# Kernel optimization log

Measured on AMD Instinct MI355X. Metric: run time of the kernel, lower is better.

Reference implementation:

```python
import jax, jax.numpy as jnp
import numpy as np

EPS = 1e-6
NEG = -100000.0


def _ln(x):
    # LayerNorm, elementwise_affine=False, eps=1e-6
    mu = jnp.mean(x, axis=-1, keepdims=True)
    var = jnp.mean((x - mu) ** 2, axis=-1, keepdims=True)
    return (x - mu) * jax.lax.rsqrt(var + EPS)


def _split_heads(x, h):
    b, s, d = x.shape
    return x.reshape(b, s, h, d // h).transpose(0, 2, 1, 3)  # [B,H,S,Dh]


def _merge_heads(x):
    b, h, s, dh = x.shape
    return x.transpose(0, 2, 1, 3).reshape(b, s, h * dh)


def _conv_pool(x, w):
    # grouped Conv2d(num_heads -> num_heads, kernel=(4,1), stride=(4,1), groups=num_heads, bias=False)
    # x: [B,H,S,Dh] as NCHW, w: [H,1,4,1] as OIHW
    return jax.lax.conv_general_dilated(
        x, w, window_strides=(4, 1), padding='VALID',
        dimension_numbers=('NCHW', 'OIHW', 'NCHW'),
        feature_group_count=x.shape[1])


def setup_inputs() -> dict:
    key = jax.random.key(0)
    ks = jax.random.split(key, 14)
    B, S, M, D, QKV, MLP, H = 4, 4096, 256, 768, 768, 3072, 12
    std = 0.02
    f = lambda k, shp: jax.random.normal(k, shp, jnp.float32) * std
    return {
        'x': jax.random.normal(ks[0], (B, S, D), jnp.float32),
        'memory': jax.random.normal(ks[1], (B, M, D), jnp.float32),
        'mask': jax.random.randint(ks[2], (B, S), 0, 2).astype(jnp.int32),
        'Wq': f(ks[3], (QKV, D)), 'Wk': f(ks[4], (QKV, D)),
        'Wv': f(ks[5], (QKV, D)), 'Wo': f(ks[6], (D, QKV)),
        'conv_w': f(ks[7], (H, 1, 4, 1)),
        'Uq': f(ks[8], (QKV, D)), 'Uk': f(ks[9], (QKV, D)),
        'Uv': f(ks[10], (QKV, D)), 'Uo': f(ks[11], (D, QKV)),
        'W1': f(ks[12], (MLP, D)), 'W2': f(ks[13], (D, MLP)),
    }


def reference(x, memory, mask, Wq, Wk, Wv, Wo, conv_w, Uq, Uk, Uv, Uo, W1, W2):
    H = conv_w.shape[0]
    maskf = mask.astype(x.dtype)                       # [B,S]

    # ---- pack: ConvAttention(memory as q, x as k/v); conv downsamples k/v ->
    #      shape_change=True so the k_mask is skipped (as in the torch code).
    q = _split_heads(memory @ Wq.T, H)                 # [B,H,M,Dh], unit temperature (log_temp=0)
    k = _split_heads(x @ Wk.T, H)                      # [B,H,S,Dh]
    v = _split_heads(x @ Wv.T, H)
    k = _conv_pool(k, conv_w)                          # [B,H,S//4,Dh]
    v = _conv_pool(v, conv_w)
    logits = jnp.einsum('bhqd,bhkd->bhqk', q, k)
    att = jax.nn.softmax(logits, axis=-1)
    packed = _merge_heads(att @ v) @ Wo.T              # [B,M,D]

    # ---- unpack: TAttention(x as q, packed as k/v) with q_mask injection
    head_dim = Uq.shape[0] // H
    uq = _split_heads(x @ Uq.T, H) * (1.0 / jnp.sqrt(jnp.asarray(head_dim, x.dtype)))
    uk = _split_heads(packed @ Uk.T, H)                # [B,H,M,Dh]
    uv = _split_heads(packed @ Uv.T, H)
    ulogits = jnp.einsum('bhqd,bhkd->bhqk', uq, uk)    # [B,H,S,M]
    ulogits = ulogits + NEG * (1.0 - maskf[:, None, :, None])
    uatt = jax.nn.softmax(ulogits, axis=-1)
    unpacked = _merge_heads(uatt @ uv) @ Uo.T          # [B,S,D]

    unpacked = unpacked * maskf[..., None]
    q_out = _ln(x + unpacked)
    m_out = _ln(memory + packed)

    # FFN: Linear -> GELU(exact) -> Linear (dropout=0)
    h = jax.nn.gelu(jnp.einsum('bsd,md->bsm', q_out, W1), approximate=False)
    y = jnp.einsum('bsm,dm->bsd', h, W2)
    y = y * maskf[..., None]
    q_out = _ln(q_out + y)
    return (q_out, m_out)
```

## Files before the change

### kernel.cpp

```cpp
#include <hip/hip_runtime.h>
#include <hip/hip_bf16.h>
#include <math.h>


typedef unsigned short u16;
typedef __attribute__((ext_vector_type(8))) short bf8v;
typedef __attribute__((ext_vector_type(4))) float f4v;
typedef __attribute__((ext_vector_type(4))) unsigned short us4v;

#define AS1 __attribute__((address_space(1)))
#define AS3 __attribute__((address_space(3)))

__device__ __forceinline__ void gld_lds16(const void* g, void* l) {
  __builtin_amdgcn_global_load_lds((const AS1 unsigned int*)g,
                                   (AS3 unsigned int*)l, 16, 0, 0);
}

__device__ __forceinline__ u16 bf16_rne(float x) {
  unsigned u = __float_as_uint(x);
  return (u16)((u + 0x7fffu + ((u >> 16) & 1u)) >> 16);
}
__device__ __forceinline__ float bf16_to_f(u16 h) {
  return __uint_as_float(((unsigned)h) << 16);
}

struct Cvt8 {
  const float* src[8];
  u16* dst[8];
  int n4[8];
  float sc[8];
  int cum[9];
  int ns;
};
__global__ __launch_bounds__(256) void tobf16_multi_kernel(Cvt8 c) {
  int b = blockIdx.x;
  int seg = 0;
  while (seg + 1 < c.ns && b >= c.cum[seg + 1]) ++seg;
  int i = (b - c.cum[seg]) * 256 + threadIdx.x;
  if (i >= c.n4[seg]) return;
  const float sc = c.sc[seg];
  float4 v = ((const float4*)c.src[seg])[i];
  us4v h;
  h[0] = bf16_rne(v.x * sc); h[1] = bf16_rne(v.y * sc);
  h[2] = bf16_rne(v.z * sc); h[3] = bf16_rne(v.w * sc);
  ((us4v*)c.dst[seg])[i] = h;
}

template <int BN, int GELU, int OMODE>
__global__ __launch_bounds__(256) void bgemm_kernel(
    const u16* __restrict__ A, const u16* __restrict__ B,
    float* __restrict__ Cf, u16* __restrict__ Cb, int M, int N, int K,
    int lda, int ldb, int ldc, long long aSB, long long aSH, long long bSB,
    long long bSH, long long cSB, long long cSH, int HB, float scale) {
  constexpr int NJ = BN / 32;
  constexpr int LPB = BN / 64;
  __shared__ u16 smA[2][4096];
  __shared__ u16 smB[2][BN * 32];
  const int t = threadIdx.x;
  const int w = t >> 6, lane = t & 63;
  const int z = blockIdx.z;
  const int bb = z / HB, hh = z % HB;
  const u16* Ab = A + bb * aSB + hh * aSH;
  const u16* Bb = B + bb * bSB + hh * bSH;
  float* Cfb = (OMODE != 1) ? (Cf + bb * cSB + hh * cSH) : nullptr;
  u16* Cbb = (OMODE >= 1) ? (Cb + bb * cSB + hh * cSH) : nullptr;

  const int gx = gridDim.x;
  const int nwg = gx * gridDim.y;
  int f = blockIdx.x + gx * blockIdx.y;
  if ((nwg & 7) == 0) {
    const int cpx = nwg >> 3;
    f = (f & 7) * cpx + (f >> 3);
  }
  const int row0 = (f / gx) * 128, col0 = (f % gx) * BN;

  const int brow_l = lane >> 2;
  const int bchunk = ((lane & 3) ^ ((lane >> 3) & 3)) * 8;
  const int fr = lane & 15;
  const int fq = lane >> 4;
  const int fco = (fq ^ ((lane >> 1) & 3)) * 8;
  const int wr = (w >> 1) * 64, wc = (w & 1) * (BN / 2);

  f4v acc[4][NJ];
#pragma unroll
  for (int i = 0; i < 4; ++i)
#pragma unroll
    for (int j = 0; j < NJ; ++j) acc[i][j] = {0.f, 0.f, 0.f, 0.f};

  const int NT = K >> 5;

#pragma unroll
  for (int i = 0; i < 2; ++i) {
    const int g = w * 2 + i;
    const int r = g * 16 + brow_l;
    gld_lds16(Ab + (long long)(row0 + r) * lda + bchunk,
              &smA[0][g * 512 + lane * 8]);
  }
#pragma unroll
  for (int i = 0; i < LPB; ++i) {
    const int g = w * LPB + i;
    const int r = g * 16 + brow_l;
    gld_lds16(Bb + (long long)(col0 + r) * ldb + bchunk,
              &smB[0][g * 512 + lane * 8]);
  }
  __syncthreads();

  for (int tt = 0; tt < NT; ++tt) {
    const int cur = tt & 1, nxt = cur ^ 1;
    const bool more = (tt + 1) < NT;
    if (more) {
      const int k1 = (tt + 1) << 5;
#pragma unroll
      for (int i = 0; i < 2; ++i) {
        const int g = w * 2 + i;
        const int r = g * 16 + brow_l;
        gld_lds16(Ab + (long long)(row0 + r) * lda + k1 + bchunk,
                  &smA[nxt][g * 512 + lane * 8]);
      }
#pragma unroll
      for (int i = 0; i < LPB; ++i) {
        const int g = w * LPB + i;
        const int r = g * 16 + brow_l;
        gld_lds16(Bb + (long long)(col0 + r) * ldb + k1 + bchunk,
                  &smB[nxt][g * 512 + lane * 8]);
      }
    }
    {
      bf8v af[4], bfr[NJ];
#pragma unroll
      for (int mi = 0; mi < 4; ++mi)
        af[mi] = *(const bf8v*)&smA[cur][(wr + mi * 16 + fr) * 32 + fco];
#pragma unroll
      for (int nj = 0; nj < NJ; ++nj)
        bfr[nj] = *(const bf8v*)&smB[cur][(wc + nj * 16 + fr) * 32 + fco];
#pragma unroll
      for (int mi = 0; mi < 4; ++mi)
#pragma unroll
        for (int nj = 0; nj < NJ; ++nj)
          acc[mi][nj] = __builtin_amdgcn_mfma_f32_16x16x32_bf16(
              af[mi], bfr[nj], acc[mi][nj], 0, 0, 0);
    }
    __syncthreads();
  }

#pragma unroll
  for (int mi = 0; mi < 4; ++mi)
#pragma unroll
    for (int nj = 0; nj < NJ; ++nj) {
      const int col = col0 + wc + nj * 16 + fr;
      const long long base =
          (long long)(row0 + wr + mi * 16 + fq * 4) * ldc + col;
#pragma unroll
      for (int j = 0; j < 4; ++j) {
        float v = acc[mi][nj][j] * scale;
        if (GELU) v = 0.5f * v * (1.f + erff(v * 0.70710678118654752f));
        const long long idx = base + (long long)j * ldc;
        if (OMODE != 1) Cfb[idx] = v;
        if (OMODE >= 1) Cbb[idx] = bf16_rne(v);
      }
    }
}

__global__ __launch_bounds__(512) void fused_pack_attn(
    const u16* __restrict__ q, const u16* __restrict__ k,
    const u16* __restrict__ vt, u16* __restrict__ o) {
  __shared__ char pool[110080];
  u16* smQ = (u16*)pool;
  u16* smK = (u16*)(pool + 16384);
  u16* Pbuf = (u16*)(pool + 32768);
  u16* smV = (u16*)(pool + 98304);
  float* partial = (float*)(pool + 106496);
  float* mold = (float*)(pool + 108544);
  float* fbuf = (float*)(pool + 109056);
  float* srow = (float*)(pool + 109568);

  const int t = threadIdx.x;
  const int w = t >> 6, lane = t & 63;
  const int z = blockIdx.z;
  const int b = z / 12, h = z % 12;
  const int qrow0 = b * 256 + blockIdx.x * 128;
  const long long kvbase = ((long long)(b * 12 + h)) * 65536;

  const int fr = lane & 15, fq = lane >> 4;
  const int fco = (fq ^ ((lane >> 1) & 3)) * 8;
  const int brow_l = lane >> 2;
  const int bchunk = ((lane & 3) ^ ((lane >> 3) & 3)) * 8;
  const int wr = (w >> 2) * 64, wc = (w & 3) * 64;
  const int wrp = (w >> 1) * 32, wcp = (w & 1) * 32;

#pragma unroll
  for (int i = 0; i < 2; ++i) {
    const int g = w * 2 + i;
    const int plane = g >> 3, grp = g & 7;
    gld_lds16(q + (long long)(qrow0 + grp * 16 + brow_l) * 768 + h * 64 +
                  plane * 32 + bchunk,
              smQ + plane * 4096 + grp * 512 + lane * 8);
  }
  if (t < 128) {
    mold[t] = -3.0e38f;
    srow[t] = 0.f;
  }

  f4v acc2[2][2];
#pragma unroll
  for (int i = 0; i < 2; ++i)
#pragma unroll
    for (int j = 0; j < 2; ++j) acc2[i][j] = {0.f, 0.f, 0.f, 0.f};

  for (int kc = 0; kc < 4; ++kc) {
    f4v acc[4][4];
#pragma unroll
    for (int i = 0; i < 4; ++i)
#pragma unroll
      for (int j = 0; j < 4; ++j) acc[i][j] = {0.f, 0.f, 0.f, 0.f};

#pragma unroll
    for (int khalf = 0; khalf < 2; ++khalf) {
      __syncthreads();
#pragma unroll
      for (int i = 0; i < 2; ++i) {
        const int g = w * 2 + i;
        gld_lds16(k + kvbase +
                      (long long)(kc * 256 + g * 16 + brow_l) * 64 +
                      khalf * 32 + bchunk,
                  smK + g * 512 + lane * 8);
      }
      __syncthreads();
#pragma unroll
      for (int mi = 0; mi < 4; ++mi) {
        const bf8v a0 =
            *(const bf8v*)&smQ[khalf * 4096 + (wr + mi * 16 + fr) * 32 + fco];
#pragma unroll
        for (int nj = 0; nj < 4; ++nj) {
          const bf8v b0 = *(const bf8v*)&smK[(wc + nj * 16 + fr) * 32 + fco];
          acc[mi][nj] =
              __builtin_amdgcn_mfma_f32_16x16x32_bf16(a0, b0, acc[mi][nj], 0, 0, 0);
        }
      }
    }
    __syncthreads();

#pragma unroll
    for (int mi = 0; mi < 4; ++mi)
#pragma unroll
      for (int j = 0; j < 4; ++j) {
        float m = fmaxf(fmaxf(acc[mi][0][j], acc[mi][1][j]),
                        fmaxf(acc[mi][2][j], acc[mi][3][j]));
#pragma unroll
        for (int o2 = 1; o2 < 16; o2 <<= 1) m = fmaxf(m, __shfl_xor(m, o2));
        if (fr == 0) partial[(w & 3) * 128 + wr + mi * 16 + fq * 4 + j] = m;
      }
    __syncthreads();
    if (t < 128) {
      const float cm = fmaxf(fmaxf(partial[t], partial[128 + t]),
                             fmaxf(partial[256 + t], partial[384 + t]));
      const float mnew = fmaxf(mold[t], cm);
      fbuf[t] = exp2f(mold[t] - mnew);
      mold[t] = mnew;
    }
    __syncthreads();

#pragma unroll
    for (int mi = 0; mi < 4; ++mi)
#pragma unroll
      for (int j = 0; j < 4; ++j) {
        const int row = wr + mi * 16 + fq * 4 + j;
        const float rm = mold[row];
        float s = 0.f;
#pragma unroll
        for (int nj = 0; nj < 4; ++nj) {
          const float e = exp2f(acc[mi][nj][j] - rm);
          s += e;
          const int col = wc + nj * 16 + fr;
          const int kc2 = col >> 5, kloc = col & 31;
          Pbuf[kc2 * 4096 + row * 32 + (((kloc >> 3) ^ ((row >> 1) & 3)) * 8) +
               (kloc & 7)] = bf16_rne(e);
        }
#pragma unroll
        for (int o2 = 1; o2 < 16; o2 <<= 1) s += __shfl_xor(s, o2);
        if (fr == 0) partial[(w & 3) * 128 + row] = s;
      }
    if (w < 4) {
      gld_lds16(vt + kvbase + (long long)(w * 16 + brow_l) * 1024 + kc * 256 +
                    bchunk,
                smV + w * 512 + lane * 8);
    }
    __syncthreads();
    if (t < 128)
      srow[t] = srow[t] * fbuf[t] +
                ((partial[t] + partial[128 + t]) +
                 (partial[256 + t] + partial[384 + t]));
    __syncthreads();

#pragma unroll
    for (int mi = 0; mi < 2; ++mi)
#pragma unroll
      for (int j = 0; j < 4; ++j) {
        const float fr_ = fbuf[wrp + mi * 16 + fq * 4 + j];
        acc2[mi][0][j] *= fr_;
        acc2[mi][1][j] *= fr_;
      }

    for (int sk = 0; sk < 8; ++sk) {
      const int cur = (sk & 1) * 2048;
      if (sk < 7 && w < 4) {
        gld_lds16(vt + kvbase + (long long)(w * 16 + brow_l) * 1024 +
                      kc * 256 + (sk + 1) * 32 + bchunk,
                  smV + (2048 - cur) + w * 512 + lane * 8);
      }
#pragma unroll
      for (int mi = 0; mi < 2; ++mi) {
        const bf8v pa =
            *(const bf8v*)&Pbuf[sk * 4096 + (wrp + mi * 16 + fr) * 32 + fco];
#pragma unroll
        for (int nj = 0; nj < 2; ++nj) {
          const bf8v v0 =
              *(const bf8v*)&smV[cur + (wcp + nj * 16 + fr) * 32 + fco];
          acc2[mi][nj] =
              __builtin_amdgcn_mfma_f32_16x16x32_bf16(pa, v0, acc2[mi][nj], 0, 0, 0);
        }
      }
      __syncthreads();
    }
  }

  if (t < 128) fbuf[t] = 1.f / srow[t];
  __syncthreads();
  const long long ooff = (long long)qrow0 * 768 + h * 64;
#pragma unroll
  for (int mi = 0; mi < 2; ++mi)
#pragma unroll
    for (int nj = 0; nj < 2; ++nj)
#pragma unroll
      for (int j = 0; j < 4; ++j) {
        const int row = wrp + mi * 16 + fq * 4 + j;
        const int col = wcp + nj * 16 + fr;
        o[ooff + (long long)row * 768 + col] =
            bf16_rne(acc2[mi][nj][j] * fbuf[row]);
      }
}

__global__ __launch_bounds__(512) void fused_unpack_attn(
    const u16* __restrict__ q, int ldq, const u16* __restrict__ k, int ldk,
    const u16* __restrict__ vt, u16* __restrict__ o) {
  __shared__ char pool[76800];
  u16* smA = (u16*)pool;
  u16* smB = (u16*)(pool + 8192);
  u16* Pbuf = (u16*)pool;
  u16* smV = (u16*)(pool + 65536);
  float* partial = (float*)(pool + 73728);
  float* rowmax = (float*)(pool + 75776);
  float* rowsum = (float*)(pool + 76288);

  const int t = threadIdx.x;
  const int w = t >> 6, lane = t & 63;
  const int z = blockIdx.z;
  const int b = z / 12, h = z % 12;
  const int q0 = blockIdx.x * 128;

  const long long qoff = (long long)(b * 4096 + q0) * ldq + h * 64;
  const long long koff = (long long)(b * 256) * ldk + h * 64;
  const long long vbase = ((long long)(b * 12 + h)) * 16384;
  const long long ooff = (long long)(b * 4096 + q0) * 768 + h * 64;

  const int fr = lane & 15, fq = lane >> 4;
  const int fco = (fq ^ ((lane >> 1) & 3)) * 8;
  const int brow_l = lane >> 2;
  const int bchunk = ((lane & 3) ^ ((lane >> 3) & 3)) * 8;

  const int wr = (w >> 2) * 64, wc = (w & 3) * 64;
  f4v acc[4][4];
#pragma unroll
  for (int i = 0; i < 4; ++i)
#pragma unroll
    for (int j = 0; j < 4; ++j) acc[i][j] = {0.f, 0.f, 0.f, 0.f};

  for (int k0 = 0; k0 < 64; k0 += 32) {
    __syncthreads();
#pragma unroll
    for (int i = 0; i < 2; ++i) {
      const int g = w * 2 + i;
      const int r = g * 16 + brow_l;
      gld_lds16(k + koff + (long long)r * ldk + k0 + bchunk,
                smB + g * 512 + lane * 8);
    }
    {
      const int r = w * 16 + brow_l;
      gld_lds16(q + qoff + (long long)r * ldq + k0 + bchunk,
                smA + w * 512 + lane * 8);
    }
    __syncthreads();
#pragma unroll
    for (int mi = 0; mi < 4; ++mi) {
      const bf8v a0 = *(const bf8v*)&smA[(wr + mi * 16 + fr) * 32 + fco];
#pragma unroll
      for (int nj = 0; nj < 4; ++nj) {
        const bf8v b0 = *(const bf8v*)&smB[(wc + nj * 16 + fr) * 32 + fco];
        acc[mi][nj] = __builtin_amdgcn_mfma_f32_16x16x32_bf16(a0, b0, acc[mi][nj], 0, 0, 0);
      }
    }
  }
  __syncthreads();

  if (w < 4) {
    const int r = w * 16 + brow_l;
    gld_lds16(vt + vbase + (long long)r * 256 + bchunk,
              smV + w * 512 + lane * 8);
  }

#pragma unroll
  for (int mi = 0; mi < 4; ++mi)
#pragma unroll
    for (int j = 0; j < 4; ++j) {
      float m = fmaxf(fmaxf(acc[mi][0][j], acc[mi][1][j]),
                      fmaxf(acc[mi][2][j], acc[mi][3][j]));
#pragma unroll
      for (int o2 = 1; o2 < 16; o2 <<= 1) m = fmaxf(m, __shfl_xor(m, o2));
      if (fr == 0) partial[(w & 3) * 128 + wr + mi * 16 + fq * 4 + j] = m;
    }
  __syncthreads();
  if (t < 128)
    rowmax[t] = fmaxf(fmaxf(partial[t], partial[128 + t]),
                      fmaxf(partial[256 + t], partial[384 + t]));
  __syncthreads();
#pragma unroll
  for (int mi = 0; mi < 4; ++mi)
#pragma unroll
    for (int j = 0; j < 4; ++j) {
      const int row = wr + mi * 16 + fq * 4 + j;
      const float rm = rowmax[row];
      float s = 0.f;
#pragma unroll
      for (int nj = 0; nj < 4; ++nj) {
        const float e = exp2f(acc[mi][nj][j] - rm);
        s += e;
        const int col = wc + nj * 16 + fr;
        const int kc = col >> 5, kloc = col & 31;
        Pbuf[kc * 4096 + row * 32 + (((kloc >> 3) ^ ((row >> 1) & 3)) * 8) +
             (kloc & 7)] = bf16_rne(e);
      }
#pragma unroll
      for (int o2 = 1; o2 < 16; o2 <<= 1) s += __shfl_xor(s, o2);
      if (fr == 0) partial[(w & 3) * 128 + row] = s;
    }
  __syncthreads();
  if (t < 128)
    rowsum[t] = 1.f / ((partial[t] + partial[128 + t]) +
                       (partial[256 + t] + partial[384 + t]));
  __syncthreads();

  const int wrp = (w >> 1) * 32, wcp = (w & 1) * 32;
  f4v acc2[2][2];
#pragma unroll
  for (int i = 0; i < 2; ++i)
#pragma unroll
    for (int j = 0; j < 2; ++j) acc2[i][j] = {0.f, 0.f, 0.f, 0.f};

  for (int kc = 0; kc < 8; ++kc) {
    const int cur = (kc & 1) * 2048;
    if (kc < 7 && w < 4) {
      const int r = w * 16 + brow_l;
      gld_lds16(vt + vbase + (long long)r * 256 + (kc + 1) * 32 + bchunk,
                smV + (2048 - cur) + w * 512 + lane * 8);
    }
#pragma unroll
    for (int mi = 0; mi < 2; ++mi) {
      const bf8v pa =
          *(const bf8v*)&Pbuf[kc * 4096 + (wrp + mi * 16 + fr) * 32 + fco];
#pragma unroll
      for (int nj = 0; nj < 2; ++nj) {
        const bf8v v0 =
            *(const bf8v*)&smV[cur + (wcp + nj * 16 + fr) * 32 + fco];
        acc2[mi][nj] = __builtin_amdgcn_mfma_f32_16x16x32_bf16(pa, v0, acc2[mi][nj], 0, 0, 0);
      }
    }
    __syncthreads();
  }
#pragma unroll
  for (int mi = 0; mi < 2; ++mi)
#pragma unroll
    for (int nj = 0; nj < 2; ++nj)
#pragma unroll
      for (int j = 0; j < 4; ++j) {
        const int row = wrp + mi * 16 + fq * 4 + j;
        const int col = wcp + nj * 16 + fr;
        o[ooff + (long long)row * 768 + col] =
            bf16_rne(acc2[mi][nj][j] * rowsum[row]);
      }
}

__global__ __launch_bounds__(256) void conv_bf16_kernel(
    const u16* __restrict__ in, const float* __restrict__ w,
    u16* __restrict__ o, int total, int ld) {
  int idx = blockIdx.x * 256 + threadIdx.x;
  if (idx >= total) return;
  const int dh = idx & 63;
  int r = idx >> 6;
  const int tt = r & 1023; r >>= 10;
  const int h = r % 12;
  const int b = r / 12;
  const long long s = ((long long)(b * 4096 + 4 * tt)) * ld + h * 64 + dh;
  const float* wh = w + h * 4;
  float v = 0.f;
#pragma unroll
  for (int j = 0; j < 4; ++j) v = fmaf(wh[j], bf16_to_f(in[s + j * ld]), v);
  o[idx] = bf16_rne(v);
}

__global__ __launch_bounds__(256) void convT_bf16_kernel(
    const u16* __restrict__ in, const float* __restrict__ w,
    u16* __restrict__ o, int total, int ld) {
  int idx = blockIdx.x * 256 + threadIdx.x;
  if (idx >= total) return;
  const int tt = idx & 1023;
  int r = idx >> 10;
  const int dh = r & 63; r >>= 6;
  const int h = r % 12;
  const int b = r / 12;
  const long long s = ((long long)(b * 4096 + 4 * tt)) * ld + h * 64 + dh;
  const float* wh = w + h * 4;
  float v = 0.f;
#pragma unroll
  for (int j = 0; j < 4; ++j) v = fmaf(wh[j], bf16_to_f(in[s + j * ld]), v);
  o[idx] = bf16_rne(v);
}

__global__ __launch_bounds__(256) void transT_b2b_kernel(
    const u16* __restrict__ in, u16* __restrict__ o, int total, int ld) {
  int idx = blockIdx.x * 256 + threadIdx.x;
  if (idx >= total) return;
  const int key = idx & 255;
  int r = idx >> 8;
  const int dh = r & 63; r >>= 6;
  const int h = r % 12;
  const int b = r / 12;
  o[idx] = in[((long long)(b * 256 + key)) * ld + h * 64 + dh];
}

__global__ __launch_bounds__(256) void ln_kernel(
    const float* __restrict__ a, const float* __restrict__ b,
    const int* __restrict__ mask, float* __restrict__ out,
    u16* __restrict__ outb) {
  const long long row = blockIdx.x;
  const float* pa = a + row * 768;
  const float* pb = b + row * 768;
  const float ms = mask ? (float)mask[row] : 1.f;
  __shared__ float buf[768];
  __shared__ float red[4];
  const int t = threadIdx.x;
  float lsum = 0.f;
#pragma unroll
  for (int i = t; i < 768; i += 256) {
    const float v = fmaf(pb[i], ms, pa[i]);
    buf[i] = v;
    lsum += v;
  }
  for (int o = 32; o; o >>= 1) lsum += __shfl_xor(lsum, o);
  if ((t & 63) == 0) red[t >> 6] = lsum;
  __syncthreads();
  const float mu = (red[0] + red[1] + red[2] + red[3]) * (1.f / 768.f);
  float lvar = 0.f;
#pragma unroll
  for (int i = t; i < 768; i += 256) {
    const float d = buf[i] - mu;
    lvar = fmaf(d, d, lvar);
  }
  __syncthreads();
  for (int o = 32; o; o >>= 1) lvar += __shfl_xor(lvar, o);
  if ((t & 63) == 0) red[t >> 6] = lvar;
  __syncthreads();
  const float var = (red[0] + red[1] + red[2] + red[3]) * (1.f / 768.f);
  const float rstd = rsqrtf(var + 1e-6f);
  float* po = out + row * 768;
  u16* pob = outb ? outb + row * 768 : nullptr;
#pragma unroll
  for (int i = t; i < 768; i += 256) {
    const float v = (buf[i] - mu) * rstd;
    po[i] = v;
    if (outb) pob[i] = bf16_rne(v);
  }
}

extern "C" void kernel_launch(void* const* d_in, const int* in_sizes, int n_in,
                              void* d_out, int out_size, void* d_ws,
                              size_t ws_size, hipStream_t stream) {
  const float* x = (const float*)d_in[0];
  const float* memory = (const float*)d_in[1];
  const int* mask = (const int*)d_in[2];
  const float* Wq = (const float*)d_in[3];
  const float* Wk = (const float*)d_in[4];
  const float* Wv = (const float*)d_in[5];
  const float* Wo = (const float*)d_in[6];
  const float* conv_w = (const float*)d_in[7];
  const float* Uq = (const float*)d_in[8];
  const float* Uk = (const float*)d_in[9];
  const float* Uv = (const float*)d_in[10];
  const float* Uo = (const float*)d_in[11];
  const float* W1 = (const float*)d_in[12];
  const float* W2 = (const float*)d_in[13];
  float* out = (float*)d_out;
  float* ws = (float*)d_ws;

  const int XR = 16384, MR = 1024, D = 768, MLP = 3072;
  const long long CB = 3145728;
  const int WD = 589824;
  const int WM = 2359296;

  float* A0 = ws + 0;
  float* A1 = ws + 18874368;
  float* A2 = ws + 31457280;

  u16* xb    = (u16*)(A0 + 12582912);
  u16* kvqb  = (u16*)A0;
  u16* uattvb = (u16*)A1;
  float* unp = A0;
  u16* qout1b = (u16*)(out + 6291456);
  u16* hb    = (u16*)A1;
  float* ybuf = A2;

  u16* kpb  = (u16*)A2;
  u16* vpTb = kpb + 3145728;
  u16* qpb  = (u16*)(A2 + 3145728);
  u16* memb = qpb + 786432;
  u16* avmb = (u16*)(A2 + 3932160);
  u16* pkb  = avmb + 786432;
  float* packed = A2 + 4718592;
  u16* ukvb = (u16*)(A2 + 5505024);
  u16* uvTb = (u16*)(A2 + 6291456);
  u16* wp16 = (u16*)(A2 + 7077888);

  u16* Wkvqb = wp16;
  u16* Wqb = wp16 + 2304 * 768;
  u16* Wob = Wqb + WD;
  u16* Ukvb2 = wp16;
  u16* Uob = wp16 + 1536 * 768;
  u16* W1b = wp16;
  u16* W2b = wp16 + WM;

  const float UQS = 0.18033688011112042592f;
  const float L2E = 1.4426950408889634074f;

  {
    Cvt8 c{};
    const float* ss[7] = {x, memory, Wk, Wv, Uq, Wq, Wo};
    u16* dd[7] = {xb, memb, Wkvqb, Wkvqb + WD, Wkvqb + 2 * WD, Wqb, Wob};
    int nn[7] = {3145728, 196608, WD / 4, WD / 4, WD / 4, WD / 4, WD / 4};
    float sc[7] = {1.f, 1.f, 1.f, 1.f, UQS, 1.f, 1.f};
    int cum = 0;
    for (int i = 0; i < 7; ++i) {
      c.src[i] = ss[i]; c.dst[i] = dd[i]; c.n4[i] = nn[i]; c.sc[i] = sc[i];
      c.cum[i] = cum; cum += (nn[i] + 255) / 256;
    }
    c.cum[7] = cum; c.ns = 7;
    tobf16_multi_kernel<<<cum, 256, 0, stream>>>(c);
  }
  bgemm_kernel<128, 0, 1><<<dim3(18, 128, 1), 256, 0, stream>>>(
      xb, Wkvqb, nullptr, kvqb, XR, 2304, D, D, D, 2304,
      0, 0, 0, 0, 0, 0, 1, 1.f);
  bgemm_kernel<128, 0, 1><<<dim3(6, 8, 1), 256, 0, stream>>>(
      memb, Wqb, nullptr, qpb, MR, D, D, D, D, D, 0, 0, 0, 0, 0, 0, 1, L2E);
  conv_bf16_kernel<<<12288, 256, 0, stream>>>(kvqb, conv_w, kpb, 3145728, 2304);
  convT_bf16_kernel<<<12288, 256, 0, stream>>>(kvqb + 768, conv_w, vpTb, 3145728, 2304);
  {
    dim3 g(2, 1, 48);
    fused_pack_attn<<<g, 512, 0, stream>>>(qpb, kpb, vpTb, avmb);
  }
  bgemm_kernel<128, 0, 2><<<dim3(6, 8, 1), 256, 0, stream>>>(
      avmb, Wob, packed, pkb, MR, D, D, D, D, D, 0, 0, 0, 0, 0, 0, 1, 1.f);
  ln_kernel<<<MR, 256, 0, stream>>>(memory, packed, nullptr, out + 12582912,
                                    nullptr);

  {
    Cvt8 c{};
    const float* ss[3] = {Uk, Uv, Uo};
    u16* dd[3] = {Ukvb2, Ukvb2 + WD, Uob};
    int cum = 0;
    for (int i = 0; i < 3; ++i) {
      c.src[i] = ss[i]; c.dst[i] = dd[i]; c.n4[i] = WD / 4; c.sc[i] = 1.f;
      c.cum[i] = cum; cum += (WD / 4 + 255) / 256;
    }
    c.cum[3] = cum; c.ns = 3;
    tobf16_multi_kernel<<<cum, 256, 0, stream>>>(c);
  }
  bgemm_kernel<128, 0, 1><<<dim3(12, 8, 1), 256, 0, stream>>>(
      pkb, Ukvb2, nullptr, ukvb, MR, 1536, D, D, D, 1536,
      0, 0, 0, 0, 0, 0, 1, 1.f);
  transT_b2b_kernel<<<3072, 256, 0, stream>>>(ukvb + 768, uvTb, 786432, 1536);
  {
    dim3 g(32, 1, 48);
    fused_unpack_attn<<<g, 512, 0, stream>>>(kvqb + 1536, 2304, ukvb, 1536,
                                             uvTb, uattvb);
  }
  bgemm_kernel<128, 0, 0><<<dim3(6, 32, 4), 256, 0, stream>>>(
      uattvb, Uob, unp, nullptr, 4096, D, D, D, D, D,
      CB, 0, 0, 0, CB, 0, 1, 1.f);
  ln_kernel<<<XR, 256, 0, stream>>>(x, unp, mask, unp, qout1b);

  {
    Cvt8 c{};
    const float* ss[2] = {W1, W2};
    u16* dd[2] = {W1b, W2b};
    int cum = 0;
    for (int i = 0; i < 2; ++i) {
      c.src[i] = ss[i]; c.dst[i] = dd[i]; c.n4[i] = WM / 4; c.sc[i] = 1.f;
      c.cum[i] = cum; cum += (WM / 4 + 255) / 256;
    }
    c.cum[2] = cum; c.ns = 2;
    tobf16_multi_kernel<<<cum, 256, 0, stream>>>(c);
  }
  for (int c = 0; c < 2; ++c) {
    bgemm_kernel<128, 1, 1><<<dim3(24, 32, 2), 256, 0, stream>>>(
        qout1b + (long long)c * 2 * CB, W1b, nullptr, hb, 4096, MLP, D,
        D, D, MLP, CB, 0, 0, 0, 12582912, 0, 1, 1.f);
    bgemm_kernel<128, 0, 0><<<dim3(6, 32, 2), 256, 0, stream>>>(
        hb, W2b, ybuf, nullptr, 4096, D, MLP, MLP, MLP, D,
        12582912, 0, 0, 0, CB, 0, 1, 1.f);
    ln_kernel<<<8192, 256, 0, stream>>>(unp + (long long)c * 2 * CB, ybuf,
                                        mask + c * 8192,
                                        out + (long long)c * 2 * CB, nullptr);
  }
}
```

Baseline: 684.2 us.

## Triple-buffer GEMM LDS pipeline with vmcnt waits; store Uo output as bf16

```diff
diff --git a/kernel.cpp b/kernel.cpp
--- a/kernel.cpp
+++ b/kernel.cpp
@@ -54,8 +54,8 @@
     long long bSH, long long cSB, long long cSH, int HB, float scale) {
   constexpr int NJ = BN / 32;
   constexpr int LPB = BN / 64;
-  __shared__ u16 smA[2][4096];
-  __shared__ u16 smB[2][BN * 32];
+  __shared__ u16 smA[3][4096];
+  __shared__ u16 smB[3][BN * 32];
   const int t = threadIdx.x;
   const int w = t >> 6, lane = t & 63;
   const int z = blockIdx.z;
@@ -89,42 +89,45 @@
 
   const int NT = K >> 5;
 
-#pragma unroll
-  for (int i = 0; i < 2; ++i) {
-    const int g = w * 2 + i;
-    const int r = g * 16 + brow_l;
-    gld_lds16(Ab + (long long)(row0 + r) * lda + bchunk,
-              &smA[0][g * 512 + lane * 8]);
-  }
-#pragma unroll
-  for (int i = 0; i < LPB; ++i) {
-    const int g = w * LPB + i;
-    const int r = g * 16 + brow_l;
-    gld_lds16(Bb + (long long)(col0 + r) * ldb + bchunk,
-              &smB[0][g * 512 + lane * 8]);
-  }
-  __syncthreads();
-
+  auto stage = [&](int tile, int buf) {
+    const int k0 = tile << 5;
+#pragma unroll
+    for (int i = 0; i < 2; ++i) {
+      const int g = w * 2 + i;
+      const int r = g * 16 + brow_l;
+      gld_lds16(Ab + (long long)(row0 + r) * lda + k0 + bchunk,
+                &smA[buf][g * 512 + lane * 8]);
+    }
+#pragma unroll
+    for (int i = 0; i < LPB; ++i) {
+      const int g = w * LPB + i;
+      const int r = g * 16 + brow_l;
+      gld_lds16(Bb + (long long)(col0 + r) * ldb + k0 + bchunk,
+                &smB[buf][g * 512 + lane * 8]);
+    }
+  };
+#define WAIT_L()                                            \
+  do {                                                      \
+    if constexpr (BN == 128)                                \
+      asm volatile("s_waitcnt vmcnt(4)" ::: "memory");      \
+    else                                                    \
+      asm volatile("s_waitcnt vmcnt(3)" ::: "memory");      \
+  } while (0)
+
+  stage(0, 0);
+  if (NT > 1) {
+    stage(1, 1);
+    WAIT_L();
+  } else {
+    asm volatile("s_waitcnt vmcnt(0)" ::: "memory");
+  }
+  __builtin_amdgcn_sched_barrier(0);
+  __builtin_amdgcn_s_barrier();
+
+  int cur = 0;
   for (int tt = 0; tt < NT; ++tt) {
-    const int cur = tt & 1, nxt = cur ^ 1;
-    const bool more = (tt + 1) < NT;
-    if (more) {
-      const int k1 = (tt + 1) << 5;
-#pragma unroll
-      for (int i = 0; i < 2; ++i) {
-        const int g = w * 2 + i;
-        const int r = g * 16 + brow_l;
-        gld_lds16(Ab + (long long)(row0 + r) * lda + k1 + bchunk,
-                  &smA[nxt][g * 512 + lane * 8]);
-      }
-#pragma unroll
-      for (int i = 0; i < LPB; ++i) {
-        const int g = w * LPB + i;
-        const int r = g * 16 + brow_l;
-        gld_lds16(Bb + (long long)(col0 + r) * ldb + k1 + bchunk,
-                  &smB[nxt][g * 512 + lane * 8]);
-      }
-    }
+    const int nn2 = (cur + 2 >= 3) ? cur - 1 : cur + 2;
+    if (tt + 2 < NT) stage(tt + 2, nn2);
     {
       bf8v af[4], bfr[NJ];
 #pragma unroll
@@ -133,15 +136,25 @@
 #pragma unroll
       for (int nj = 0; nj < NJ; ++nj)
         bfr[nj] = *(const bf8v*)&smB[cur][(wc + nj * 16 + fr) * 32 + fco];
+      __builtin_amdgcn_s_setprio(1);
 #pragma unroll
       for (int mi = 0; mi < 4; ++mi)
 #pragma unroll
         for (int nj = 0; nj < NJ; ++nj)
           acc[mi][nj] = __builtin_amdgcn_mfma_f32_16x16x32_bf16(
               af[mi], bfr[nj], acc[mi][nj], 0, 0, 0);
-    }
-    __syncthreads();
-  }
+      __builtin_amdgcn_s_setprio(0);
+    }
+    if (tt + 2 < NT) {
+      WAIT_L();
+    } else if (tt + 1 < NT) {
+      asm volatile("s_waitcnt vmcnt(0)" ::: "memory");
+    }
+    __builtin_amdgcn_sched_barrier(0);
+    __builtin_amdgcn_s_barrier();
+    cur = (cur + 1 >= 3) ? 0 : cur + 1;
+  }
+#undef WAIT_L
 
 #pragma unroll
   for (int mi = 0; mi < 4; ++mi)
@@ -537,13 +550,13 @@
   o[idx] = in[((long long)(b * 256 + key)) * ld + h * 64 + dh];
 }
 
+template <int BBF16>
 __global__ __launch_bounds__(256) void ln_kernel(
-    const float* __restrict__ a, const float* __restrict__ b,
-    const int* __restrict__ mask, float* __restrict__ out,
-    u16* __restrict__ outb) {
+    const float* __restrict__ a, const float* __restrict__ bf,
+    const u16* __restrict__ bb, const int* __restrict__ mask,
+    float* __restrict__ out, u16* __restrict__ outb) {
   const long long row = blockIdx.x;
   const float* pa = a + row * 768;
-  const float* pb = b + row * 768;
   const float ms = mask ? (float)mask[row] : 1.f;
   __shared__ float buf[768];
   __shared__ float red[4];
@@ -551,7 +564,8 @@
   float lsum = 0.f;
 #pragma unroll
   for (int i = t; i < 768; i += 256) {
-    const float v = fmaf(pb[i], ms, pa[i]);
+    const float bvv = BBF16 ? bf16_to_f(bb[row * 768 + i]) : bf[row * 768 + i];
+    const float v = fmaf(bvv, ms, pa[i]);
     buf[i] = v;
     lsum += v;
   }
@@ -613,7 +627,8 @@
   u16* xb    = (u16*)(A0 + 12582912);
   u16* kvqb  = (u16*)A0;
   u16* uattvb = (u16*)A1;
-  float* unp = A0;
+  u16* unpb  = (u16*)A0;
+  float* qout1 = A0 + 6291456;
   u16* qout1b = (u16*)(out + 6291456);
   u16* hb    = (u16*)A1;
   float* ybuf = A2;
@@ -667,8 +682,8 @@
   }
   bgemm_kernel<128, 0, 2><<<dim3(6, 8, 1), 256, 0, stream>>>(
       avmb, Wob, packed, pkb, MR, D, D, D, D, D, 0, 0, 0, 0, 0, 0, 1, 1.f);
-  ln_kernel<<<MR, 256, 0, stream>>>(memory, packed, nullptr, out + 12582912,
-                                    nullptr);
+  ln_kernel<0><<<MR, 256, 0, stream>>>(memory, packed, nullptr, nullptr,
+                                       out + 12582912, nullptr);
 
   {
     Cvt8 c{};
@@ -691,10 +706,10 @@
     fused_unpack_attn<<<g, 512, 0, stream>>>(kvqb + 1536, 2304, ukvb, 1536,
                                              uvTb, uattvb);
   }
-  bgemm_kernel<128, 0, 0><<<dim3(6, 32, 4), 256, 0, stream>>>(
-      uattvb, Uob, unp, nullptr, 4096, D, D, D, D, D,
+  bgemm_kernel<128, 0, 1><<<dim3(6, 32, 4), 256, 0, stream>>>(
+      uattvb, Uob, nullptr, unpb, 4096, D, D, D, D, D,
       CB, 0, 0, 0, CB, 0, 1, 1.f);
-  ln_kernel<<<XR, 256, 0, stream>>>(x, unp, mask, unp, qout1b);
+  ln_kernel<1><<<XR, 256, 0, stream>>>(x, nullptr, unpb, mask, qout1, qout1b);
 
   {
     Cvt8 c{};
@@ -715,8 +730,8 @@
     bgemm_kernel<128, 0, 0><<<dim3(6, 32, 2), 256, 0, stream>>>(
         hb, W2b, ybuf, nullptr, 4096, D, MLP, MLP, MLP, D,
         12582912, 0, 0, 0, CB, 0, 1, 1.f);
-    ln_kernel<<<8192, 256, 0, stream>>>(unp + (long long)c * 2 * CB, ybuf,
-                                        mask + c * 8192,
-                                        out + (long long)c * 2 * CB, nullptr);
-  }
-}
+    ln_kernel<0><<<8192, 256, 0, stream>>>(qout1 + (long long)c * 2 * CB, ybuf,
+                                           nullptr, mask + c * 8192,
+                                           out + (long long)c * 2 * CB, nullptr);
+  }
+}
```

Result: no change. 687.2 us (+0.4%).
